# Performance work log

Hardware: AMD Instinct MI355X
Metric: run time of the kernel (lower is better)

The kernel has to match this reference:

```python
import jax, jax.numpy as jnp
import numpy as np

ATTRACTION_W = 1.0
REPULSION_W = 1.0
MARGIN = 0.3  # hardcoded local `margin = 0.3` in the torch forward


def setup_inputs() -> dict:
    key = jax.random.key(0)
    k1, k2, k3 = jax.random.split(key, 3)
    B, N, D, K = 16, 65536, 32, 512
    beta = jax.random.normal(k1, (B, N, 1), dtype=jnp.float32)
    embed = jax.random.normal(k2, (B, N, D), dtype=jnp.float32)
    # instance id per hit: -1 = background, 0..K-1 = instances
    sid = jax.random.randint(k3, (B, N), -1, K).astype(jnp.int32)
    # first K hits are the condensation points, one per instance
    sid = sid.at[:, :K].set(jnp.arange(K, dtype=jnp.int32)[None, :])
    is_cp = jnp.zeros((B, N), dtype=jnp.int32).at[:, :K].set(1)
    return {"beta": beta, "embed": embed, "slice_id": sid, "is_cp": is_cp, "num_instances": K}


def _per_batch(beta_b, emb_b, sid, iscp, K):
    # beta_b: [N], emb_b: [N, D], sid/iscp: [N]
    N = sid.shape[0]
    cp = iscp == 1
    valid = sid >= 0
    noncp = valid & ~cp  # non-cp signal hits
    pos = cp.sum().astype(jnp.float32)
    neg = jnp.float32(N) - pos  # noncp + background
    pos_w = jax.lax.stop_gradient(neg / (pos + 1e-6))
    w = jnp.where(cp, pos_w, jnp.where(noncp, 1.0, 2.0))
    # weighted BCE-with-logits, reduction='mean'
    x = beta_b
    y = cp.astype(jnp.float32)
    bce = jnp.maximum(x, 0.0) - x * y + jnp.log1p(jnp.exp(-jnp.abs(x)))
    beta_ce = (w * bce).mean()

    # segment id: valid hits -> sid, background -> dummy segment K (dropped)
    seg = jnp.where(valid, sid, K)
    counts = jax.ops.segment_sum(valid.astype(jnp.float32), seg, num_segments=K + 1)[:K]
    inst_exists = counts > 0  # the `unique()` set

    # first cp hit index per instance (sentinel N if instance has no cp)
    idxs = jnp.arange(N)
    first_cp = jax.ops.segment_min(jnp.where(cp & valid, idxs, N), seg, num_segments=K + 1)[:K]
    has_cp = first_cp < N
    safe_cp = jnp.minimum(first_cp, N - 1)
    cp_emb = emb_b[safe_cp]  # [K, D]
    cp_beta = beta_b[safe_cp]  # [K]

    # attraction: sum over instances (with a cp) of mean ||e_hit - e_cp||^2
    sid_c = jnp.clip(sid, 0, K - 1)
    d2 = ((emb_b - cp_emb[sid_c]) ** 2).sum(-1)  # [N]
    d2 = jnp.where(valid, d2, 0.0)
    seg_d2 = jax.ops.segment_sum(d2, seg, num_segments=K + 1)[:K]
    attr = (jnp.where(has_cp & inst_exists, seg_d2 / jnp.maximum(counts, 1.0), 0.0).sum()
            * ATTRACTION_W)

    # ranking: instances with exactly 1 cp and >0 noncp hits
    cp_count = jax.ops.segment_sum((cp & valid).astype(jnp.float32), seg, num_segments=K + 1)[:K]
    ncp_count = jax.ops.segment_sum(noncp.astype(jnp.float32), seg, num_segments=K + 1)[:K]
    r = jax.nn.relu(beta_b + MARGIN - cp_beta[sid_c])
    r = jnp.where(noncp, r, 0.0)
    seg_r = jax.ops.segment_sum(r, seg, num_segments=K + 1)[:K]
    qual = (cp_count == 1.0) & (ncp_count > 0)
    n_unique = inst_exists.sum().astype(jnp.float32)
    ranking = (jnp.where(qual, seg_r / jnp.maximum(ncp_count, 1.0), 0.0).sum()
               / jnp.maximum(n_unique, 1.0))

    beta_loss = beta_ce + 2.0 * ranking

    # repulsion over all cp hits; data has exactly one cp per instance so the
    # cp set equals cp_emb (K points), matching torch's emb_b[cp_idx]
    diff = cp_emb[:, None, :] - cp_emb[None, :, :]  # [K, K, D]
    rep = jnp.exp(-(diff ** 2).sum(-1)).mean() * REPULSION_W

    return beta_loss + attr + rep, beta_loss, attr, rep


def reference(beta, embed, slice_id, is_cp, num_instances):
    K = int(num_instances)
    beta2 = beta[..., 0]  # squeeze(-1)
    loss_b, bl, al, rl = jax.vmap(lambda b, e, s, c: _per_batch(b, e, s, c, K))(
        beta2, embed, slice_id, is_cp)
    return loss_b.mean(), bl.mean(), al.mean(), rl.mean()
```

## Files before the change

kernel.cpp:

```cpp
#include <hip/hip_runtime.h>
#include <math.h>

#define N_HITS 65536
#define K_INST 512
#define MARGIN 0.3f
#define BPB    128
#define HITS_PB (N_HITS / BPB)

__device__ __forceinline__ unsigned short f2bf(float f) {
    unsigned u = __float_as_uint(f);
    return (unsigned short)((u + 0x7FFFu + ((u >> 16) & 1u)) >> 16);
}
__device__ __forceinline__ float bf2f(unsigned short h) {
    return __uint_as_float(((unsigned)h) << 16);
}

__global__ __launch_bounds__(256) void k_scan(
    const int* __restrict__ sid, const int* __restrict__ iscp,
    int* first_cp, int* pos_cnt) {
    int b = blockIdx.y;
    size_t bo = (size_t)b * N_HITS;
    int i = blockIdx.x * 256 + threadIdx.x;
    int stride = gridDim.x * 256;
    for (; i < N_HITS; i += stride) {
        int c = iscp[bo + i];
        if (c == 1) {
            atomicAdd(&pos_cnt[b], 1);
            int s = sid[bo + i];
            if (s >= 0) atomicMin(&first_cp[b * K_INST + s], i);
        }
    }
}

__global__ __launch_bounds__(256) void k_gather(
    const float* __restrict__ beta, const float4* __restrict__ embed4,
    const int* __restrict__ first_cp,
    float* cp_beta, float4* cp_emb4, ushort4* cpb_g, int B) {
    int g = blockIdx.x * 256 + threadIdx.x;
    int total = B * K_INST * 8;
    if (g >= total) return;
    int row = g >> 3, sub = g & 7;
    int b = row / K_INST;
    int fc = first_cp[row];
    int safe = min(fc, N_HITS - 1);
    float4 e = embed4[((size_t)b * N_HITS + safe) * 8 + sub];
    cp_emb4[(size_t)row * 8 + sub] = e;
    ushort4 h;
    h.x = f2bf(e.x); h.y = f2bf(e.y); h.z = f2bf(e.z); h.w = f2bf(e.w);
    cpb_g[(size_t)row * 8 + (sub ^ (row & 7))] = h;
    if (sub == 0) cp_beta[row] = beta[b * N_HITS + safe];
}

__global__ __launch_bounds__(256) void k_main(
    const float*  __restrict__ beta,
    const float4* __restrict__ embed4,
    const int*    __restrict__ sid_g, const int* __restrict__ iscp_g,
    const ushort4* __restrict__ cpb_g, const float* __restrict__ cp_beta,
    int* cnt_packed, float* seg_d2, float* seg_r,
    float* s_cp, float* s_ncp, float* s_bg) {
    __shared__ ushort4 cpb[K_INST * 8];
    __shared__ float   d2p[K_INST * 4];
    __shared__ int     l_cnt[K_INST];
    __shared__ float   l_r[K_INST];
    __shared__ float   l_cb[K_INST];
    __shared__ float   l_red[12];

    int b = blockIdx.y, tid = threadIdx.x;
    size_t bo = (size_t)b * N_HITS;
    int base = blockIdx.x * HITS_PB;

    for (int k = tid; k < K_INST; k += 256) {
        l_cnt[k] = 0; l_r[k] = 0.f;
        l_cb[k] = cp_beta[b * K_INST + k];
    }
    for (int k = tid; k < K_INST * 4; k += 256) d2p[k] = 0.f;
    {
        const ushort4* src = cpb_g + (size_t)b * K_INST * 8;
        for (int k = tid; k < K_INST * 8; k += 256) cpb[k] = src[k];
    }
    __syncthreads();

    float a_cp = 0.f, a_ncp = 0.f, a_bg = 0.f;
#pragma unroll
    for (int h = 0; h < HITS_PB / 256; ++h) {
        int i = base + h * 256 + tid;
        int s = sid_g[bo + i];
        int c = iscp_g[bo + i];
        float x = beta[bo + i];
        bool cp = (c == 1), valid = (s >= 0), noncp = valid && !cp;
        float t = __expf(-fabsf(x));
        float bce = fmaxf(x, 0.f) - (cp ? x : 0.f) + __logf(1.f + t);
        if (cp) a_cp += bce; else if (noncp) a_ncp += bce; else a_bg += bce;
        if (valid) {
            atomicAdd(&l_cnt[s], cp ? (1 << 20) : 1);
            if (noncp) {
                float r = fmaxf(x + MARGIN - l_cb[s], 0.f);
                atomicAdd(&l_r[s], r);
            }
        }
    }

    {
        int sub = tid & 7, hgrp = tid >> 3;
#pragma unroll 4
        for (int it = 0; it < HITS_PB / 32; ++it) {
            int i = base + it * 32 + hgrp;
            int s = sid_g[bo + i];
            float4 e = embed4[(bo + i) * 8 + sub];
            int sc = min(max(s, 0), K_INST - 1);
            ushort4 h = cpb[sc * 8 + (sub ^ (sc & 7))];
            float c0 = bf2f(h.x), c1 = bf2f(h.y), c2 = bf2f(h.z), c3 = bf2f(h.w);
            float q = e.x * (e.x - 2.f * c0) + e.y * (e.y - 2.f * c1)
                    + e.z * (e.z - 2.f * c2) + e.w * (e.w - 2.f * c3);
            if (s >= 0) atomicAdd(&d2p[sc * 4 + (sub & 3)], q);
        }
    }

    for (int o = 32; o > 0; o >>= 1) {
        a_cp  += __shfl_down(a_cp, o);
        a_ncp += __shfl_down(a_ncp, o);
        a_bg  += __shfl_down(a_bg, o);
    }
    int wave = tid >> 6;
    if ((tid & 63) == 0) { l_red[wave] = a_cp; l_red[4 + wave] = a_ncp; l_red[8 + wave] = a_bg; }
    __syncthreads();
    if (tid == 0) {
        atomicAdd(&s_cp[b],  l_red[0] + l_red[1] + l_red[2]  + l_red[3]);
        atomicAdd(&s_ncp[b], l_red[4] + l_red[5] + l_red[6]  + l_red[7]);
        atomicAdd(&s_bg[b],  l_red[8] + l_red[9] + l_red[10] + l_red[11]);
    }
    for (int k = tid; k < K_INST; k += 256) {
        int   cv = l_cnt[k]; if (cv) atomicAdd(&cnt_packed[b * K_INST + k], cv);
        float dv = d2p[k * 4] + d2p[k * 4 + 1] + d2p[k * 4 + 2] + d2p[k * 4 + 3];
        if (dv != 0.f) atomicAdd(&seg_d2[b * K_INST + k], dv);
        float rv = l_r[k]; if (rv != 0.f) atomicAdd(&seg_r[b * K_INST + k], rv);
    }
}

__global__ __launch_bounds__(512) void k_tail(
    const float4* __restrict__ cp_emb4, const ushort4* __restrict__ cpb_g,
    const int* __restrict__ cnt_packed, const float* __restrict__ seg_d2,
    const float* __restrict__ seg_r, const int* __restrict__ first_cp,
    const int* __restrict__ pos_cnt, const float* __restrict__ s_cp,
    const float* __restrict__ s_ncp, const float* __restrict__ s_bg,
    float* attr_b, float* rank_b, float* nuniq_b, float* rep_b,
    int* ctr, float* out, int B) {
    int tid = threadIdx.x;
    int nrep = B * 16;

    if ((int)blockIdx.x < nrep) {
        __shared__ float4 tile[32 * 8];
        __shared__ float red[8];
        int b = blockIdx.x >> 4, t2 = blockIdx.x & 15;
        const float4* base = cp_emb4 + (size_t)b * K_INST * 8;
        float4 r0[8];
#pragma unroll
        for (int cc = 0; cc < 8; ++cc) r0[cc] = base[(size_t)tid * 8 + cc];
        if (tid < 256) tile[tid] = base[(size_t)t2 * 256 + tid];
        __syncthreads();
        float acc = 0.f;
        for (int j = 0; j < 32; ++j) {
            float d2 = 0.f;
#pragma unroll
            for (int cc = 0; cc < 8; ++cc) {
                float4 ev = tile[j * 8 + cc];
                float ax = r0[cc].x - ev.x, ay = r0[cc].y - ev.y;
                float az = r0[cc].z - ev.z, aw = r0[cc].w - ev.w;
                d2 += ax * ax + ay * ay + az * az + aw * aw;
            }
            acc += __expf(-d2);
        }
        for (int o = 32; o > 0; o >>= 1) acc += __shfl_down(acc, o);
        if ((tid & 63) == 0) red[tid >> 6] = acc;
        __syncthreads();
        if (tid == 0) {
            float t = 0.f;
            for (int w = 0; w < 8; ++w) t += red[w];
            atomicAdd(&rep_b[b], t);
        }
    } else {
        __shared__ float red2[3][8];
        int b = blockIdx.x - nrep, k = tid;
        int v = cnt_packed[b * K_INST + k];
        int ncp = v & 0xFFFFF, cpc = v >> 20;
        int counts = ncp + cpc;
        int fc = first_cp[b * K_INST + k];
        bool has_cp = fc < N_HITS, exists = counts > 0;
        const ushort4* cq = cpb_g + ((size_t)b * K_INST + k) * 8;
        float s2 = 0.f;
#pragma unroll
        for (int j = 0; j < 8; ++j) {
            ushort4 h = cq[j];
            float c0 = bf2f(h.x), c1 = bf2f(h.y), c2 = bf2f(h.z), c3 = bf2f(h.w);
            s2 += c0 * c0 + c1 * c1 + c2 * c2 + c3 * c3;
        }
        float segd = seg_d2[b * K_INST + k] + (float)counts * s2;
        float attr = (has_cp && exists) ? segd / fmaxf((float)counts, 1.f) : 0.f;
        float rank = (cpc == 1 && ncp > 0) ? seg_r[b * K_INST + k] / fmaxf((float)ncp, 1.f) : 0.f;
        float uq = exists ? 1.f : 0.f;
        for (int o = 32; o > 0; o >>= 1) {
            attr += __shfl_down(attr, o);
            rank += __shfl_down(rank, o);
            uq   += __shfl_down(uq, o);
        }
        if ((k & 63) == 0) { red2[0][k >> 6] = attr; red2[1][k >> 6] = rank; red2[2][k >> 6] = uq; }
        __syncthreads();
        if (k == 0) {
            float a = 0.f, r = 0.f, u = 0.f;
            for (int w = 0; w < 8; ++w) { a += red2[0][w]; r += red2[1][w]; u += red2[2][w]; }
            attr_b[b] = a; rank_b[b] = r; nuniq_b[b] = u;
        }
    }

    __shared__ int is_last;
    __syncthreads();
    if (tid == 0) {
        __threadfence();
        int v = atomicAdd(ctr, 1);
        is_last = (v == (int)gridDim.x - 1);
    }
    __syncthreads();
    if (is_last) {
        __threadfence();
        if (tid < 64) {
            int b = tid;
            float loss = 0.f, bl = 0.f, at = 0.f, rp = 0.f;
            if (b < B) {
                float pos = (float)pos_cnt[b];
                float pw = ((float)N_HITS - pos) / (pos + 1e-6f);
                float bce = (pw * s_cp[b] + s_ncp[b] + 2.f * s_bg[b]) / (float)N_HITS;
                float rank = rank_b[b] / fmaxf(nuniq_b[b], 1.f);
                bl = bce + 2.f * rank;
                at = attr_b[b];
                rp = rep_b[b] / (float)(K_INST * K_INST);
                loss = bl + at + rp;
            }
            for (int o = 32; o > 0; o >>= 1) {
                loss += __shfl_down(loss, o);
                bl   += __shfl_down(bl, o);
                at   += __shfl_down(at, o);
                rp   += __shfl_down(rp, o);
            }
            if (tid == 0) {
                float inv = 1.f / (float)B;
                out[0] = loss * inv;
                out[1] = bl * inv;
                out[2] = at * inv;
                out[3] = rp * inv;
            }
        }
    }
}

extern "C" void kernel_launch(void* const* d_in, const int* in_sizes, int n_in,
                              void* d_out, int out_size, void* d_ws, size_t ws_size,
                              hipStream_t stream) {
    const float*  beta   = (const float*)d_in[0];
    const float*  embed  = (const float*)d_in[1];
    const int*    sid    = (const int*)d_in[2];
    const int*    iscp   = (const int*)d_in[3];
    float* out = (float*)d_out;

    int BN = in_sizes[0];
    int B  = BN / N_HITS;
    int BK = B * K_INST;

    char* ws = (char*)d_ws;
    int*   cnt_packed = (int*)ws;
    float* seg_d2     = (float*)(ws + 4 * (size_t)BK);
    float* seg_r      = (float*)(ws + 8 * (size_t)BK);
    float* scal       = (float*)(ws + 12 * (size_t)BK);
    int*   pos_cnt  = (int*)scal;
    float* s_cp     = scal + 1 * B;
    float* s_ncp    = scal + 2 * B;
    float* s_bg     = scal + 3 * B;
    float* attr_b   = scal + 4 * B;
    float* rank_b   = scal + 5 * B;
    float* nuniq_b  = scal + 6 * B;
    float* rep_b    = scal + 7 * B;
    int*   ctr      = (int*)(scal + 8 * B);
    size_t zbytes = 12 * (size_t)BK + 32 * (size_t)B + 16;
    int*     first_cp = (int*)(ws + zbytes);
    float*   cp_beta  = (float*)(ws + zbytes + 4 * (size_t)BK);
    float4*  cp_emb4  = (float4*)(ws + zbytes + 8 * (size_t)BK);
    ushort4* cpb_g    = (ushort4*)(ws + zbytes + 8 * (size_t)BK + 128 * (size_t)BK);

    hipMemsetAsync(ws, 0, zbytes, stream);
    hipMemsetAsync(first_cp, 0x7F, 4 * (size_t)BK, stream);

    k_scan<<<dim3(32, B), 256, 0, stream>>>(sid, iscp, first_cp, pos_cnt);

    k_gather<<<(BK * 8 + 255) / 256, 256, 0, stream>>>(beta, (const float4*)embed,
                                                       first_cp, cp_beta, cp_emb4,
                                                       cpb_g, B);

    k_main<<<dim3(BPB, B), 256, 0, stream>>>(beta, (const float4*)embed, sid, iscp,
                                             (const ushort4*)cpb_g, cp_beta,
                                             cnt_packed, seg_d2, seg_r,
                                             s_cp, s_ncp, s_bg);

    k_tail<<<B * 16 + B, 512, 0, stream>>>(cp_emb4, (const ushort4*)cpb_g,
                                           cnt_packed, seg_d2, seg_r,
                                           first_cp, pos_cnt, s_cp, s_ncp, s_bg,
                                           attr_b, rank_b, nuniq_b, rep_b,
                                           ctr, out, B);
}
```

Before: 297.7 us.

## Drop LDS cp table, cache sids in LDS, use per-block partials with reduce kernel

The main kernel no longer copies the per-batch bf16 condensation-point table into shared memory and instead reads it directly from global memory (L2-resident). This cuts LDS use and raises the occupancy hint to 8 blocks per CU. Slice ids from the first pass are kept in shared memory as shorts so the second pass does not reload them. When workspace allows, per-block segment partials are written out and summed by a new reduce kernel instead of global atomics. The costs are an extra launch, extra partial-buffer traffic, and possibly uncoalesced global gathers for the cp table.

```diff
diff --git a/kernel.cpp b/kernel.cpp
--- a/kernel.cpp
+++ b/kernel.cpp
@@ -47,23 +47,24 @@
     cp_emb4[(size_t)row * 8 + sub] = e;
     ushort4 h;
     h.x = f2bf(e.x); h.y = f2bf(e.y); h.z = f2bf(e.z); h.w = f2bf(e.w);
-    cpb_g[(size_t)row * 8 + (sub ^ (row & 7))] = h;
+    cpb_g[(size_t)row * 8 + sub] = h;
     if (sub == 0) cp_beta[row] = beta[b * N_HITS + safe];
 }
 
-__global__ __launch_bounds__(256) void k_main(
+__global__ __launch_bounds__(256, 8) void k_main(
     const float*  __restrict__ beta,
     const float4* __restrict__ embed4,
     const int*    __restrict__ sid_g, const int* __restrict__ iscp_g,
     const ushort4* __restrict__ cpb_g, const float* __restrict__ cp_beta,
+    int* pc_cnt, float* pc_d2, float* pc_r,
     int* cnt_packed, float* seg_d2, float* seg_r,
-    float* s_cp, float* s_ncp, float* s_bg) {
-    __shared__ ushort4 cpb[K_INST * 8];
-    __shared__ float   d2p[K_INST * 4];
-    __shared__ int     l_cnt[K_INST];
-    __shared__ float   l_r[K_INST];
-    __shared__ float   l_cb[K_INST];
-    __shared__ float   l_red[12];
+    float* s_cp, float* s_ncp, float* s_bg, int use_part) {
+    __shared__ float d2p[K_INST * 4];
+    __shared__ int   l_cnt[K_INST];
+    __shared__ float l_r[K_INST];
+    __shared__ float l_cb[K_INST];
+    __shared__ short st_s[HITS_PB];
+    __shared__ float l_red[12];
 
     int b = blockIdx.y, tid = threadIdx.x;
     size_t bo = (size_t)b * N_HITS;
@@ -74,42 +75,39 @@
         l_cb[k] = cp_beta[b * K_INST + k];
     }
     for (int k = tid; k < K_INST * 4; k += 256) d2p[k] = 0.f;
-    {
-        const ushort4* src = cpb_g + (size_t)b * K_INST * 8;
-        for (int k = tid; k < K_INST * 8; k += 256) cpb[k] = src[k];
-    }
     __syncthreads();
 
     float a_cp = 0.f, a_ncp = 0.f, a_bg = 0.f;
 #pragma unroll
     for (int h = 0; h < HITS_PB / 256; ++h) {
-        int i = base + h * 256 + tid;
+        int idx = h * 256 + tid;
+        int i = base + idx;
         int s = sid_g[bo + i];
         int c = iscp_g[bo + i];
         float x = beta[bo + i];
+        st_s[idx] = (short)s;
         bool cp = (c == 1), valid = (s >= 0), noncp = valid && !cp;
         float t = __expf(-fabsf(x));
         float bce = fmaxf(x, 0.f) - (cp ? x : 0.f) + __logf(1.f + t);
         if (cp) a_cp += bce; else if (noncp) a_ncp += bce; else a_bg += bce;
         if (valid) {
             atomicAdd(&l_cnt[s], cp ? (1 << 20) : 1);
-            if (noncp) {
-                float r = fmaxf(x + MARGIN - l_cb[s], 0.f);
-                atomicAdd(&l_r[s], r);
-            }
-        }
-    }
+            if (noncp) atomicAdd(&l_r[s], fmaxf(x + MARGIN - l_cb[s], 0.f));
+        }
+    }
+    __syncthreads();
 
     {
         int sub = tid & 7, hgrp = tid >> 3;
+        const ushort4* cpt = cpb_g + (size_t)b * K_INST * 8;
 #pragma unroll 4
         for (int it = 0; it < HITS_PB / 32; ++it) {
-            int i = base + it * 32 + hgrp;
-            int s = sid_g[bo + i];
-            float4 e = embed4[(bo + i) * 8 + sub];
-            int sc = min(max(s, 0), K_INST - 1);
-            ushort4 h = cpb[sc * 8 + (sub ^ (sc & 7))];
-            float c0 = bf2f(h.x), c1 = bf2f(h.y), c2 = bf2f(h.z), c3 = bf2f(h.w);
+            int hit = it * 32 + hgrp;
+            int s = st_s[hit];
+            float4 e = embed4[(bo + base + hit) * 8 + sub];
+            int sc = max(s, 0);
+            ushort4 hh = cpt[(size_t)sc * 8 + sub];
+            float c0 = bf2f(hh.x), c1 = bf2f(hh.y), c2 = bf2f(hh.z), c3 = bf2f(hh.w);
             float q = e.x * (e.x - 2.f * c0) + e.y * (e.y - 2.f * c1)
                     + e.z * (e.z - 2.f * c2) + e.w * (e.w - 2.f * c3);
             if (s >= 0) atomicAdd(&d2p[sc * 4 + (sub & 3)], q);
@@ -129,11 +127,46 @@
         atomicAdd(&s_ncp[b], l_red[4] + l_red[5] + l_red[6]  + l_red[7]);
         atomicAdd(&s_bg[b],  l_red[8] + l_red[9] + l_red[10] + l_red[11]);
     }
-    for (int k = tid; k < K_INST; k += 256) {
-        int   cv = l_cnt[k]; if (cv) atomicAdd(&cnt_packed[b * K_INST + k], cv);
-        float dv = d2p[k * 4] + d2p[k * 4 + 1] + d2p[k * 4 + 2] + d2p[k * 4 + 3];
-        if (dv != 0.f) atomicAdd(&seg_d2[b * K_INST + k], dv);
-        float rv = l_r[k]; if (rv != 0.f) atomicAdd(&seg_r[b * K_INST + k], rv);
+    if (use_part) {
+        size_t po = ((size_t)b * BPB + blockIdx.x) * K_INST;
+        for (int k = tid; k < K_INST; k += 256) {
+            pc_cnt[po + k] = l_cnt[k];
+            pc_d2[po + k]  = d2p[k * 4] + d2p[k * 4 + 1] + d2p[k * 4 + 2] + d2p[k * 4 + 3];
+            pc_r[po + k]   = l_r[k];
+        }
+    } else {
+        for (int k = tid; k < K_INST; k += 256) {
+            int cv = l_cnt[k]; if (cv) atomicAdd(&cnt_packed[b * K_INST + k], cv);
+            float dv = d2p[k * 4] + d2p[k * 4 + 1] + d2p[k * 4 + 2] + d2p[k * 4 + 3];
+            if (dv != 0.f) atomicAdd(&seg_d2[b * K_INST + k], dv);
+            float rv = l_r[k]; if (rv != 0.f) atomicAdd(&seg_r[b * K_INST + k], rv);
+        }
+    }
+}
+
+__global__ __launch_bounds__(256) void k_reduce(
+    const int* __restrict__ pc_cnt, const float* __restrict__ pc_d2,
+    const float* __restrict__ pc_r,
+    int* cnt_packed, float* seg_d2, float* seg_r) {
+    __shared__ int   rc[4][64];
+    __shared__ float rd[4][64];
+    __shared__ float rr[4][64];
+    int kl = threadIdx.x & 63, p4 = threadIdx.x >> 6;
+    int bin = blockIdx.x * 64 + kl;
+    int b = bin / K_INST;
+    size_t basep = ((size_t)b * BPB) * K_INST + (bin % K_INST);
+    int cs = 0; float ds = 0.f, rs = 0.f;
+    for (int p = p4 * (BPB / 4); p < (p4 + 1) * (BPB / 4); ++p) {
+        cs += pc_cnt[basep + (size_t)p * K_INST];
+        ds += pc_d2[basep + (size_t)p * K_INST];
+        rs += pc_r[basep + (size_t)p * K_INST];
+    }
+    rc[p4][kl] = cs; rd[p4][kl] = ds; rr[p4][kl] = rs;
+    __syncthreads();
+    if (p4 == 0) {
+        cnt_packed[bin] = rc[0][kl] + rc[1][kl] + rc[2][kl] + rc[3][kl];
+        seg_d2[bin]     = rd[0][kl] + rd[1][kl] + rd[2][kl] + rd[3][kl];
+        seg_r[bin]      = rr[0][kl] + rr[1][kl] + rr[2][kl] + rr[3][kl];
     }
 }
 
@@ -284,6 +317,13 @@
     float*   cp_beta  = (float*)(ws + zbytes + 4 * (size_t)BK);
     float4*  cp_emb4  = (float4*)(ws + zbytes + 8 * (size_t)BK);
     ushort4* cpb_g    = (ushort4*)(ws + zbytes + 8 * (size_t)BK + 128 * (size_t)BK);
+    char*    partbase = ws + zbytes + 8 * (size_t)BK + 128 * (size_t)BK + 64 * (size_t)BK;
+    size_t   psz      = (size_t)B * BPB * K_INST * 4;
+    int*     pc_cnt   = (int*)partbase;
+    float*   pc_d2    = (float*)(partbase + psz);
+    float*   pc_r     = (float*)(partbase + 2 * psz);
+    size_t   need     = (size_t)(partbase - ws) + 3 * psz;
+    int use_part = (ws_size >= need) ? 1 : 0;
 
     hipMemsetAsync(ws, 0, zbytes, stream);
     hipMemsetAsync(first_cp, 0x7F, 4 * (size_t)BK, stream);
@@ -296,8 +336,13 @@
 
     k_main<<<dim3(BPB, B), 256, 0, stream>>>(beta, (const float4*)embed, sid, iscp,
                                              (const ushort4*)cpb_g, cp_beta,
+                                             pc_cnt, pc_d2, pc_r,
                                              cnt_packed, seg_d2, seg_r,
-                                             s_cp, s_ncp, s_bg);
+                                             s_cp, s_ncp, s_bg, use_part);
+
+    if (use_part)
+        k_reduce<<<BK / 64, 256, 0, stream>>>(pc_cnt, pc_d2, pc_r,
+                                              cnt_packed, seg_d2, seg_r);
 
     k_tail<<<B * 16 + B, 512, 0, stream>>>(cp_emb4, (const ushort4*)cpb_g,
                                            cnt_packed, seg_d2, seg_r,
```

Measured after the change: 276.9 us. -7.0%, faster.
